# Kernel optimization log

Measured on AMD Instinct MI355X. Metric: run time of the kernel, lower is better.

## Reference

```python
import jax, jax.numpy as jnp
import numpy as np

EPS = 1e-6
NUM_HEADS = 16

def rmsnorm(x, w):
    # x: [..., d], w: [d]
    norm = jax.lax.rsqrt(jnp.mean(x * x, axis=-1, keepdims=True) + EPS)
    return w * (x * norm)

def setup_inputs() -> dict:
    key = jax.random.key(0)
    ks = jax.random.split(key, 6)
    B, N, C = 2, 2048, 1024
    H = NUM_HEADS
    hd = C // H
    x = jax.random.normal(ks[0], (B, N, C), dtype=jnp.float32)
    scale = 1.0 / np.sqrt(C)
    qkv_w = jax.random.normal(ks[1], (C, 3 * C), dtype=jnp.float32) * scale
    qkv_b = jnp.zeros((3 * C,), dtype=jnp.float32)
    q_norm_w = jnp.ones((hd,), dtype=jnp.float32)
    k_norm_w = jnp.ones((hd,), dtype=jnp.float32)
    proj_w = jax.random.normal(ks[2], (C, C), dtype=jnp.float32) * scale
    proj_b = jnp.zeros((C,), dtype=jnp.float32)
    return {"x": x, "qkv_w": qkv_w, "qkv_b": qkv_b,
            "q_norm_w": q_norm_w, "k_norm_w": k_norm_w,
            "proj_w": proj_w, "proj_b": proj_b}

def reference(x, qkv_w, qkv_b, q_norm_w, k_norm_w, proj_w, proj_b):
    B, N, C = x.shape
    H = NUM_HEADS
    hd = C // H
    qkv = x @ qkv_w + qkv_b                       # [B,N,3C]
    qkv = qkv.reshape(B, N, 3, H, hd)
    q, k, v = qkv[:, :, 0], qkv[:, :, 1], qkv[:, :, 2]  # [B,N,H,hd]
    q = jnp.transpose(q, (0, 2, 1, 3))            # [B,H,N,hd]
    k = jnp.transpose(k, (0, 2, 1, 3))
    v = jnp.transpose(v, (0, 2, 1, 3))
    q = rmsnorm(q, q_norm_w)
    k = rmsnorm(k, k_norm_w)
    scores = jnp.einsum('bhqd,bhkd->bhqk', q, k) / jnp.sqrt(jnp.float32(hd))
    attn = jax.nn.softmax(scores, axis=-1)
    out = jnp.einsum('bhqk,bhkd->bhqd', attn, v)  # [B,H,N,hd]
    out = jnp.transpose(out, (0, 2, 1, 3)).reshape(B, N, C)
    return out @ proj_w + proj_b
```

## Files before the change

### kernel.cpp

```cpp
#include <hip/hip_runtime.h>

typedef unsigned short u16;
typedef unsigned int u32;
typedef __bf16 bf16x8 __attribute__((ext_vector_type(8)));
typedef float f32x4 __attribute__((ext_vector_type(4)));
typedef unsigned short u16x8 __attribute__((ext_vector_type(8)));
typedef unsigned short u16x4 __attribute__((ext_vector_type(4)));

__device__ __forceinline__ float bf2f(u16 u) {
    union { unsigned int i; float f; } c; c.i = ((unsigned int)u) << 16; return c.f;
}
__device__ __forceinline__ u16 f2bf(float f) {
    union { float f; unsigned int i; } c; c.f = f;
    unsigned int r = c.i + 0x7FFFu + ((c.i >> 16) & 1u);
    return (u16)(r >> 16);
}
__device__ __forceinline__ u16 f2bf_rtz(float f) {
    union { float f; unsigned int i; } c; c.f = f;
    return (u16)(c.i >> 16);
}
__device__ __forceinline__ float fast_exp2(float x) {
#if __has_builtin(__builtin_amdgcn_exp2f)
    return __builtin_amdgcn_exp2f(x);
#else
    return exp2f(x);
#endif
}
__device__ __forceinline__ bf16x8 u2b(u16x8 v) {
    return __builtin_bit_cast(bf16x8, v);
}
__device__ __forceinline__ void async16(const void* g, void* l) {
    __builtin_amdgcn_global_load_lds(
        (const __attribute__((address_space(1))) u32*)g,
        (__attribute__((address_space(3))) u32*)l, 16, 0, 0);
}

__global__ __launch_bounds__(256) void prep(
    const float* __restrict__ X, u16* __restrict__ Xb,
    const float* __restrict__ qkv_w, u16* __restrict__ qwT,
    const float* __restrict__ proj_w, u16* __restrict__ pwT)
{
    __shared__ float tile[32][33];
    const int blk = blockIdx.x;
    const int t = threadIdx.x;
    if (blk < 2048) {
        const size_t i = ((size_t)blk * 256 + t) * 8;
        u16x8 h;
        #pragma unroll
        for (int e = 0; e < 8; ++e) h[e] = f2bf(X[i + e]);
        *(u16x8*)&Xb[i] = h;
        return;
    }
    const float* W; u16* Th; int K, N, bx, by;
    if (blk < 5120) {
        W = qkv_w; Th = qwT; K = 1024; N = 3072;
        bx = (blk - 2048) % 96; by = (blk - 2048) / 96;
    } else {
        W = proj_w; Th = pwT; K = 1024; N = 1024;
        bx = (blk - 5120) % 32; by = (blk - 5120) / 32;
    }
    const int bk = by * 32, bn = bx * 32;
    const int tx = t & 31, ty = t >> 5;
    #pragma unroll
    for (int r = ty; r < 32; r += 8)
        tile[r][tx] = W[(size_t)(bk + r) * N + bn + tx];
    __syncthreads();
    #pragma unroll
    for (int r = ty; r < 32; r += 8)
        Th[(size_t)(bn + r) * K + bk + tx] = f2bf(tile[tx][r]);
}

__global__ __launch_bounds__(256) void gemm_qkv(
    const u16* __restrict__ AH, const u16* __restrict__ BH,
    const float* __restrict__ bias,
    u16* __restrict__ Qb, u16* __restrict__ Kb, u16* __restrict__ Vt,
    const float* __restrict__ qw, const float* __restrict__ kw)
{
    const int K = 1024;
    __shared__ __align__(16) u16 AhT[128 * 32];
    __shared__ __align__(16) u16 BhT[128 * 32];
    const int t = threadIdx.x;
    const int bm = blockIdx.y * 128, bn = blockIdx.x * 128;
    const int wave = t >> 6, lane = t & 63;
    const int wm = (wave >> 1) * 64, wn = (wave & 1) * 64;
    const int l15 = lane & 15, quad = lane >> 4;
    const int srow = lane >> 2;
    const int scol = (((lane & 3) ^ ((lane >> 3) & 3))) * 8;
    const int rq = (quad ^ ((l15 >> 1) & 3)) * 8;

    f32x4 acc[4][4];
    const f32x4 zero = {0.0f, 0.0f, 0.0f, 0.0f};
    #pragma unroll
    for (int i = 0; i < 4; ++i)
        #pragma unroll
        for (int j = 0; j < 4; ++j) acc[i][j] = zero;

    for (int k0 = 0; k0 < K; k0 += 32) {
        #pragma unroll
        for (int rr = 0; rr < 2; ++rr) {
            const int r0 = (rr * 4 + wave) * 16;
            const size_t ga = (size_t)(bm + r0 + srow) * K + k0 + scol;
            const size_t gb = (size_t)(bn + r0 + srow) * K + k0 + scol;
            async16(&AH[ga], &AhT[r0 * 32]);
            async16(&BH[gb], &BhT[r0 * 32]);
        }
        __syncthreads();
        bf16x8 ah[4], bh[4];
        #pragma unroll
        for (int i = 0; i < 4; ++i)
            ah[i] = *(const bf16x8*)&AhT[(wm + i * 16 + l15) * 32 + rq];
        #pragma unroll
        for (int j = 0; j < 4; ++j)
            bh[j] = *(const bf16x8*)&BhT[(wn + j * 16 + l15) * 32 + rq];
        #pragma unroll
        for (int i = 0; i < 4; ++i)
            #pragma unroll
            for (int j = 0; j < 4; ++j)
                acc[i][j] = __builtin_amdgcn_mfma_f32_16x16x32_bf16(
                    ah[i], bh[j], acc[i][j], 0, 0, 0);
        __syncthreads();
    }

    const int gc0 = bn + wn;
    const int sec = gc0 >> 10;
    const int h = (gc0 & 1023) >> 6;
    const int b = bm >> 11;
    const int bhd = b * 16 + h;
    float bv[4], wj[4];
    #pragma unroll
    for (int j = 0; j < 4; ++j) {
        const int d = j * 16 + l15;
        bv[j] = bias[gc0 + d];
        wj[j] = (sec == 2) ? 0.0f : (sec ? kw[d] : qw[d] * 0.18033688011f);
    }
    if (sec < 2) {
        u16* dst = sec ? Kb : Qb;
        #pragma unroll
        for (int i = 0; i < 4; ++i) {
            float val[4][4];
            float ss[4] = {0.0f, 0.0f, 0.0f, 0.0f};
            #pragma unroll
            for (int j = 0; j < 4; ++j)
                #pragma unroll
                for (int r = 0; r < 4; ++r) {
                    val[j][r] = acc[i][j][r] + bv[j];
                    ss[r] += val[j][r] * val[j][r];
                }
            #pragma unroll
            for (int r = 0; r < 4; ++r) {
                #pragma unroll
                for (int m = 1; m < 16; m <<= 1)
                    ss[r] += __shfl_xor(ss[r], m, 64);
                const float nrm = rsqrtf(ss[r] * 0.015625f + 1e-6f);
                const int n = (bm + wm + i * 16 + quad * 4 + r) & 2047;
                const size_t rowb = ((size_t)bhd * 2048 + n) * 64;
                #pragma unroll
                for (int j = 0; j < 4; ++j)
                    dst[rowb + j * 16 + l15] = f2bf(val[j][r] * nrm * wj[j]);
            }
        }
    } else {
        const int nb = (bm + wm) & 2047;
        #pragma unroll
        for (int i = 0; i < 4; ++i) {
            const int s0 = (i & 1) * 32 + quad * 8 + (i >> 1) * 4;
            #pragma unroll
            for (int j = 0; j < 4; ++j) {
                const int d = j * 16 + l15;
                u16x4 pk;
                #pragma unroll
                for (int r = 0; r < 4; ++r)
                    pk[r] = f2bf(acc[i][j][r] + bv[j]);
                *(u16x4*)&Vt[((size_t)bhd * 64 + d) * 2048 + nb + s0] = pk;
            }
        }
    }
}

__global__ __launch_bounds__(256) void gemm_proj(
    const u16* __restrict__ AH, const u16* __restrict__ BH,
    const float* __restrict__ bias, float* __restrict__ C)
{
    const int N = 1024, K = 1024;
    __shared__ __align__(16) u16 AhT[64 * 32];
    __shared__ __align__(16) u16 BhT[128 * 32];
    const int t = threadIdx.x;
    const int bm = blockIdx.y * 64, bn = blockIdx.x * 128;
    const int wave = t >> 6, lane = t & 63;
    const int l15 = lane & 15, quad = lane >> 4;
    const int srow = lane >> 2;
    const int scol = (((lane & 3) ^ ((lane >> 3) & 3))) * 8;
    const int rq = (quad ^ ((l15 >> 1) & 3)) * 8;

    f32x4 acc[4][2];
    const f32x4 zero = {0.0f, 0.0f, 0.0f, 0.0f};
    #pragma unroll
    for (int i = 0; i < 4; ++i)
        #pragma unroll
        for (int j = 0; j < 2; ++j) acc[i][j] = zero;

    for (int k0 = 0; k0 < K; k0 += 32) {
        {
            const int r0 = wave * 16;
            async16(&AH[(size_t)(bm + r0 + srow) * K + k0 + scol],
                    &AhT[r0 * 32]);
        }
        #pragma unroll
        for (int cc = 0; cc < 2; ++cc) {
            const int r0 = (wave * 2 + cc) * 16;
            async16(&BH[(size_t)(bn + r0 + srow) * K + k0 + scol],
                    &BhT[r0 * 32]);
        }
        __syncthreads();
        bf16x8 ah[4], bh[2];
        #pragma unroll
        for (int i = 0; i < 4; ++i)
            ah[i] = *(const bf16x8*)&AhT[(i * 16 + l15) * 32 + rq];
        #pragma unroll
        for (int j = 0; j < 2; ++j)
            bh[j] = *(const bf16x8*)
                &BhT[(wave * 32 + j * 16 + l15) * 32 + rq];
        #pragma unroll
        for (int i = 0; i < 4; ++i)
            #pragma unroll
            for (int j = 0; j < 2; ++j)
                acc[i][j] = __builtin_amdgcn_mfma_f32_16x16x32_bf16(
                    ah[i], bh[j], acc[i][j], 0, 0, 0);
        __syncthreads();
    }

    #pragma unroll
    for (int j = 0; j < 2; ++j) {
        const int col = bn + wave * 32 + j * 16 + l15;
        const float bv = bias[col];
        #pragma unroll
        for (int i = 0; i < 4; ++i) {
            const int row = bm + i * 16 + quad * 4;
            #pragma unroll
            for (int r = 0; r < 4; ++r)
                C[(size_t)(row + r) * N + col] = acc[i][j][r] + bv;
        }
    }
}

__global__ __launch_bounds__(256) void flash_attn_mfma(
    const u16* __restrict__ Qb, const u16* __restrict__ Kb,
    const u16* __restrict__ Vt, u16* __restrict__ Attn)
{
    __shared__ __align__(16) u16 Klds[2 * 64 * 64];
    __shared__ __align__(16) u16 Vlds[2 * 64 * 64];

    const int t = threadIdx.x;
    const int bid = blockIdx.x;
    const int bh = bid & 31;
    const int qt = bid >> 5;
    const int n0 = qt * 128;
    const size_t kbase = (size_t)bh * 2048 * 64;
    const size_t vbase = (size_t)bh * 64 * 2048;
    const int wave = t >> 6, lane = t & 63;
    const int l15 = lane & 15, quad = lane >> 4;
    const int srow8 = lane >> 3;
    const int sgrp = lane & 7;

    bf16x8 qf[2][2];
    #pragma unroll
    for (int qs = 0; qs < 2; ++qs) {
        const size_t qrow =
            ((size_t)bh * 2048 + n0 + wave * 32 + qs * 16 + l15) * 64;
        qf[qs][0] = *(const bf16x8*)&Qb[qrow + quad * 8];
        qf[qs][1] = *(const bf16x8*)&Qb[qrow + 32 + quad * 8];
    }

    int kofs[4][2];
    #pragma unroll
    for (int nt = 0; nt < 4; ++nt) {
        const int row = nt * 16 + l15;
        kofs[nt][0] = row * 64 + ((quad ^ (row & 7)) * 8);
        kofs[nt][1] = row * 64 + (((quad + 4) ^ (row & 7)) * 8);
    }

    f32x4 o[2][4];
    const f32x4 zero = {0.0f, 0.0f, 0.0f, 0.0f};
    #pragma unroll
    for (int qs = 0; qs < 2; ++qs)
        #pragma unroll
        for (int dt = 0; dt < 4; ++dt) o[qs][dt] = zero;
    f32x4 osum[2] = {zero, zero};
    bf16x8 ones;
    #pragma unroll
    for (int e = 0; e < 8; ++e) ones[e] = (__bf16)1.0f;

    #pragma unroll
    for (int cc = 0; cc < 2; ++cc) {
        const int r0 = (wave + cc * 4) * 8;
        const int row = r0 + srow8;
        const int gg = sgrp ^ (row & 7);
        async16(&Kb[kbase + (size_t)row * 64 + gg * 8], &Klds[r0 * 64]);
        async16(&Vt[vbase + (size_t)row * 2048 + gg * 8], &Vlds[r0 * 64]);
    }

    for (int kt = 0; kt < 32; ++kt) {
        __syncthreads();
        if (kt + 1 < 32) {
            const int nb = ((kt + 1) & 1) * 4096;
            #pragma unroll
            for (int cc = 0; cc < 2; ++cc) {
                const int r0 = (wave + cc * 4) * 8;
                const int row = r0 + srow8;
                const int gg = sgrp ^ (row & 7);
                async16(&Kb[kbase + (size_t)((kt + 1) * 64 + row) * 64 + gg * 8],
                        &Klds[nb + r0 * 64]);
                async16(&Vt[vbase + (size_t)row * 2048 + (kt + 1) * 64 + gg * 8],
                        &Vlds[nb + r0 * 64]);
            }
        }
        const int cb = (kt & 1) * 4096;

        f32x4 s[2][4];
        #pragma unroll
        for (int nt = 0; nt < 4; ++nt) {
            bf16x8 kf0 = *(const bf16x8*)&Klds[cb + kofs[nt][0]];
            bf16x8 kf1 = *(const bf16x8*)&Klds[cb + kofs[nt][1]];
            __builtin_amdgcn_s_setprio(1);
            #pragma unroll
            for (int qs = 0; qs < 2; ++qs) {
                s[qs][nt] = __builtin_amdgcn_mfma_f32_16x16x32_bf16(
                    kf0, qf[qs][0], zero, 0, 0, 0);
                s[qs][nt] = __builtin_amdgcn_mfma_f32_16x16x32_bf16(
                    kf1, qf[qs][1], s[qs][nt], 0, 0, 0);
            }
            __builtin_amdgcn_s_setprio(0);
        }

        bf16x8 pf[2][2];
        #pragma unroll
        for (int qs = 0; qs < 2; ++qs) {
            #pragma unroll
            for (int m = 0; m < 2; ++m) {
                u16x8 pk;
                #pragma unroll
                for (int r = 0; r < 4; ++r) {
                    pk[r]     = f2bf_rtz(fast_exp2(s[qs][m][r]));
                    pk[4 + r] = f2bf_rtz(fast_exp2(s[qs][m + 2][r]));
                }
                pf[qs][m] = u2b(pk);
            }
        }

        #pragma unroll
        for (int dt = 0; dt < 4; ++dt) {
            bf16x8 vf0 = *(const bf16x8*)&Vlds[cb + kofs[dt][0]];
            bf16x8 vf1 = *(const bf16x8*)&Vlds[cb + kofs[dt][1]];
            __builtin_amdgcn_s_setprio(1);
            #pragma unroll
            for (int qs = 0; qs < 2; ++qs) {
                o[qs][dt] = __builtin_amdgcn_mfma_f32_16x16x32_bf16(
                    pf[qs][0], vf0, o[qs][dt], 0, 0, 0);
                o[qs][dt] = __builtin_amdgcn_mfma_f32_16x16x32_bf16(
                    pf[qs][1], vf1, o[qs][dt], 0, 0, 0);
            }
            __builtin_amdgcn_s_setprio(0);
        }
        __builtin_amdgcn_s_setprio(1);
        #pragma unroll
        for (int qs = 0; qs < 2; ++qs) {
            osum[qs] = __builtin_amdgcn_mfma_f32_16x16x32_bf16(
                pf[qs][0], ones, osum[qs], 0, 0, 0);
            osum[qs] = __builtin_amdgcn_mfma_f32_16x16x32_bf16(
                pf[qs][1], ones, osum[qs], 0, 0, 0);
        }
        __builtin_amdgcn_s_setprio(0);
    }

    const size_t obase =
        ((size_t)(bh >> 4) * 2048 + n0) * 1024 + (bh & 15) * 64;
    #pragma unroll
    for (int qs = 0; qs < 2; ++qs)
        #pragma unroll
        for (int r = 0; r < 4; ++r) {
            const float inv = 1.0f / osum[qs][r];
            const size_t rbase =
                obase + (size_t)(wave * 32 + qs * 16 + quad * 4 + r) * 1024;
            #pragma unroll
            for (int dt = 0; dt < 4; ++dt)
                Attn[rbase + dt * 16 + l15] = f2bf(o[qs][dt][r] * inv);
        }
}

extern "C" void kernel_launch(void* const* d_in, const int* in_sizes, int n_in,
                              void* d_out, int out_size, void* d_ws, size_t ws_size,
                              hipStream_t stream)
{
    const float* x      = (const float*)d_in[0];
    const float* qkv_w  = (const float*)d_in[1];
    const float* qkv_b  = (const float*)d_in[2];
    const float* q_nw   = (const float*)d_in[3];
    const float* k_nw   = (const float*)d_in[4];
    const float* proj_w = (const float*)d_in[5];
    const float* proj_b = (const float*)d_in[6];
    float* out = (float*)d_out;

    char* ws = (char*)d_ws;
    u16* AttnB = (u16*)ws;
    u16* qwT   = (u16*)(ws + 8388608);
    u16* pwT   = (u16*)(ws + 14680064);
    u16* Xb    = (u16*)(ws + 16777216);
    u16* QbB   = (u16*)(ws + 25165824);
    u16* KbB   = (u16*)(ws + 33554432);
    u16* VtB   = (u16*)(ws + 41943040);
    (void)in_sizes; (void)n_in; (void)out_size;
    if (ws_size < 50331648u) return;

    prep<<<dim3(6144), 256, 0, stream>>>(x, Xb, qkv_w, qwT, proj_w, pwT);
    gemm_qkv<<<dim3(3072 / 128, 4096 / 128), 256, 0, stream>>>(
        Xb, qwT, qkv_b, QbB, KbB, VtB, q_nw, k_nw);
    flash_attn_mfma<<<dim3(512), 256, 0, stream>>>(QbB, KbB, VtB, AttnB);
    gemm_proj<<<dim3(1024 / 128, 4096 / 64), 256, 0, stream>>>(
        AttnB, pwT, proj_b, out);
}
```

Baseline: 198.7 us.

## Double QKV GEMM k-tile to 64 and remap blocks for XCD locality

The QKV GEMM now loads 64-wide K slices per iteration into larger LDS tiles with a new XOR swizzle, halving the number of barrier pairs per K loop. It also replaces the 2D grid with a 1D grid of 768 blocks, mapping each XCD to a contiguous set of column tiles so weight tiles are more likely to be reused in that XCD's L2. The price is doubled LDS usage and more live registers for the fragments, which could lower occupancy.

```diff
diff --git a/kernel.cpp b/kernel.cpp
--- a/kernel.cpp
+++ b/kernel.cpp
@@ -77,16 +77,19 @@
     const float* __restrict__ qw, const float* __restrict__ kw)
 {
     const int K = 1024;
-    __shared__ __align__(16) u16 AhT[128 * 32];
-    __shared__ __align__(16) u16 BhT[128 * 32];
+    __shared__ __align__(16) u16 AhT[128 * 64];
+    __shared__ __align__(16) u16 BhT[128 * 64];
     const int t = threadIdx.x;
-    const int bm = blockIdx.y * 128, bn = blockIdx.x * 128;
+    const int bid = blockIdx.x;
+    const int xcd = bid & 7, slot = bid >> 3;
+    const int bm = (slot / 3) * 128;
+    const int bn = (xcd * 3 + (slot % 3)) * 128;
     const int wave = t >> 6, lane = t & 63;
     const int wm = (wave >> 1) * 64, wn = (wave & 1) * 64;
     const int l15 = lane & 15, quad = lane >> 4;
-    const int srow = lane >> 2;
-    const int scol = (((lane & 3) ^ ((lane >> 3) & 3))) * 8;
-    const int rq = (quad ^ ((l15 >> 1) & 3)) * 8;
+    const int srow_lo = lane >> 3;
+    const int g8 = ((lane & 7) ^ (lane >> 3)) * 8;
+    const int rx = l15 & 7;
 
     f32x4 acc[4][4];
     const f32x4 zero = {0.0f, 0.0f, 0.0f, 0.0f};
@@ -95,29 +98,37 @@
         #pragma unroll
         for (int j = 0; j < 4; ++j) acc[i][j] = zero;
 
-    for (int k0 = 0; k0 < K; k0 += 32) {
-        #pragma unroll
-        for (int rr = 0; rr < 2; ++rr) {
-            const int r0 = (rr * 4 + wave) * 16;
-            const size_t ga = (size_t)(bm + r0 + srow) * K + k0 + scol;
-            const size_t gb = (size_t)(bn + r0 + srow) * K + k0 + scol;
-            async16(&AH[ga], &AhT[r0 * 32]);
-            async16(&BH[gb], &BhT[r0 * 32]);
+    for (int k0 = 0; k0 < K; k0 += 64) {
+        #pragma unroll
+        for (int cc = 0; cc < 4; ++cc) {
+            const int seg = cc * 4 + wave;
+            const int row = seg * 8 + srow_lo;
+            async16(&AH[(size_t)(bm + row) * K + k0 + g8], &AhT[seg * 512]);
+            async16(&BH[(size_t)(bn + row) * K + k0 + g8], &BhT[seg * 512]);
         }
         __syncthreads();
-        bf16x8 ah[4], bh[4];
+        bf16x8 ah[4][2], bh[4][2];
+        #pragma unroll
+        for (int i = 0; i < 4; ++i) {
+            const int rb = (wm + i * 16 + l15) * 64;
+            ah[i][0] = *(const bf16x8*)&AhT[rb + (quad ^ rx) * 8];
+            ah[i][1] = *(const bf16x8*)&AhT[rb + (((4 + quad) ^ rx)) * 8];
+        }
+        #pragma unroll
+        for (int j = 0; j < 4; ++j) {
+            const int rb = (wn + j * 16 + l15) * 64;
+            bh[j][0] = *(const bf16x8*)&BhT[rb + (quad ^ rx) * 8];
+            bh[j][1] = *(const bf16x8*)&BhT[rb + (((4 + quad) ^ rx)) * 8];
+        }
         #pragma unroll
         for (int i = 0; i < 4; ++i)
-            ah[i] = *(const bf16x8*)&AhT[(wm + i * 16 + l15) * 32 + rq];
-        #pragma unroll
-        for (int j = 0; j < 4; ++j)
-            bh[j] = *(const bf16x8*)&BhT[(wn + j * 16 + l15) * 32 + rq];
-        #pragma unroll
-        for (int i = 0; i < 4; ++i)
-            #pragma unroll
-            for (int j = 0; j < 4; ++j)
+            #pragma unroll
+            for (int j = 0; j < 4; ++j) {
                 acc[i][j] = __builtin_amdgcn_mfma_f32_16x16x32_bf16(
-                    ah[i], bh[j], acc[i][j], 0, 0, 0);
+                    ah[i][0], bh[j][0], acc[i][j], 0, 0, 0);
+                acc[i][j] = __builtin_amdgcn_mfma_f32_16x16x32_bf16(
+                    ah[i][1], bh[j][1], acc[i][j], 0, 0, 0);
+            }
         __syncthreads();
     }
 
@@ -412,7 +423,7 @@
     if (ws_size < 50331648u) return;
 
     prep<<<dim3(6144), 256, 0, stream>>>(x, Xb, qkv_w, qwT, proj_w, pwT);
-    gemm_qkv<<<dim3(3072 / 128, 4096 / 128), 256, 0, stream>>>(
+    gemm_qkv<<<dim3(768), 256, 0, stream>>>(
         Xb, qwT, qkv_b, QbB, KbB, VtB, q_nw, k_nw);
     flash_attn_mfma<<<dim3(512), 256, 0, stream>>>(QbB, KbB, VtB, AttnB);
     gemm_proj<<<dim3(1024 / 128, 4096 / 64), 256, 0, stream>>>(
```

Measured after the change: 198.2 us. No clear change (-0.3%).

## Double K-step per barrier in proj GEMM and drop setprio in attention

Applied to the files above, without the earlier changes.

The projection GEMM now loads two 32-wide K slices into LDS per iteration, halving the number of __syncthreads barriers and loop iterations at the cost of double the shared memory. Separately, the s_setprio priority hints around the MFMA blocks in the flash attention kernel are removed. Both changes aim to reduce synchronization and scheduling overhead. Removing setprio may change how waves interleave memory and compute.

```diff
diff --git a/kernel.cpp b/kernel.cpp
--- a/kernel.cpp
+++ b/kernel.cpp
@@ -182,8 +182,8 @@
     const float* __restrict__ bias, float* __restrict__ C)
 {
     const int N = 1024, K = 1024;
-    __shared__ __align__(16) u16 AhT[64 * 32];
-    __shared__ __align__(16) u16 BhT[128 * 32];
+    __shared__ __align__(16) u16 AhT[2 * 64 * 32];
+    __shared__ __align__(16) u16 BhT[2 * 128 * 32];
     const int t = threadIdx.x;
     const int bm = blockIdx.y * 64, bn = blockIdx.x * 128;
     const int wave = t >> 6, lane = t & 63;
@@ -199,33 +199,41 @@
         #pragma unroll
         for (int j = 0; j < 2; ++j) acc[i][j] = zero;
 
-    for (int k0 = 0; k0 < K; k0 += 32) {
-        {
-            const int r0 = wave * 16;
-            async16(&AH[(size_t)(bm + r0 + srow) * K + k0 + scol],
-                    &AhT[r0 * 32]);
-        }
-        #pragma unroll
-        for (int cc = 0; cc < 2; ++cc) {
-            const int r0 = (wave * 2 + cc) * 16;
-            async16(&BH[(size_t)(bn + r0 + srow) * K + k0 + scol],
-                    &BhT[r0 * 32]);
+    for (int k0 = 0; k0 < K; k0 += 64) {
+        #pragma unroll
+        for (int s = 0; s < 2; ++s) {
+            const int kk = k0 + s * 32;
+            {
+                const int r0 = wave * 16;
+                async16(&AH[(size_t)(bm + r0 + srow) * K + kk + scol],
+                        &AhT[s * 2048 + r0 * 32]);
+            }
+            #pragma unroll
+            for (int cc = 0; cc < 2; ++cc) {
+                const int r0 = (wave * 2 + cc) * 16;
+                async16(&BH[(size_t)(bn + r0 + srow) * K + kk + scol],
+                        &BhT[s * 4096 + r0 * 32]);
+            }
         }
         __syncthreads();
-        bf16x8 ah[4], bh[2];
-        #pragma unroll
-        for (int i = 0; i < 4; ++i)
-            ah[i] = *(const bf16x8*)&AhT[(i * 16 + l15) * 32 + rq];
-        #pragma unroll
-        for (int j = 0; j < 2; ++j)
-            bh[j] = *(const bf16x8*)
-                &BhT[(wave * 32 + j * 16 + l15) * 32 + rq];
-        #pragma unroll
-        for (int i = 0; i < 4; ++i)
+        #pragma unroll
+        for (int s = 0; s < 2; ++s) {
+            const int ab = s * 2048, bb = s * 4096;
+            bf16x8 ah[4], bh[2];
+            #pragma unroll
+            for (int i = 0; i < 4; ++i)
+                ah[i] = *(const bf16x8*)&AhT[ab + (i * 16 + l15) * 32 + rq];
             #pragma unroll
             for (int j = 0; j < 2; ++j)
-                acc[i][j] = __builtin_amdgcn_mfma_f32_16x16x32_bf16(
-                    ah[i], bh[j], acc[i][j], 0, 0, 0);
+                bh[j] = *(const bf16x8*)
+                    &BhT[bb + (wave * 32 + j * 16 + l15) * 32 + rq];
+            #pragma unroll
+            for (int i = 0; i < 4; ++i)
+                #pragma unroll
+                for (int j = 0; j < 2; ++j)
+                    acc[i][j] = __builtin_amdgcn_mfma_f32_16x16x32_bf16(
+                        ah[i], bh[j], acc[i][j], 0, 0, 0);
+        }
         __syncthreads();
     }
 
@@ -321,7 +329,6 @@
         for (int nt = 0; nt < 4; ++nt) {
             bf16x8 kf0 = *(const bf16x8*)&Klds[cb + kofs[nt][0]];
             bf16x8 kf1 = *(const bf16x8*)&Klds[cb + kofs[nt][1]];
-            __builtin_amdgcn_s_setprio(1);
             #pragma unroll
             for (int qs = 0; qs < 2; ++qs) {
                 s[qs][nt] = __builtin_amdgcn_mfma_f32_16x16x32_bf16(
@@ -329,7 +336,6 @@
                 s[qs][nt] = __builtin_amdgcn_mfma_f32_16x16x32_bf16(
                     kf1, qf[qs][1], s[qs][nt], 0, 0, 0);
             }
-            __builtin_amdgcn_s_setprio(0);
         }
 
         bf16x8 pf[2][2];
@@ -351,7 +357,6 @@
         for (int dt = 0; dt < 4; ++dt) {
             bf16x8 vf0 = *(const bf16x8*)&Vlds[cb + kofs[dt][0]];
             bf16x8 vf1 = *(const bf16x8*)&Vlds[cb + kofs[dt][1]];
-            __builtin_amdgcn_s_setprio(1);
             #pragma unroll
             for (int qs = 0; qs < 2; ++qs) {
                 o[qs][dt] = __builtin_amdgcn_mfma_f32_16x16x32_bf16(
@@ -359,9 +364,7 @@
                 o[qs][dt] = __builtin_amdgcn_mfma_f32_16x16x32_bf16(
                     pf[qs][1], vf1, o[qs][dt], 0, 0, 0);
             }
-            __builtin_amdgcn_s_setprio(0);
-        }
-        __builtin_amdgcn_s_setprio(1);
+        }
         #pragma unroll
         for (int qs = 0; qs < 2; ++qs) {
             osum[qs] = __builtin_amdgcn_mfma_f32_16x16x32_bf16(
@@ -369,7 +372,6 @@
             osum[qs] = __builtin_amdgcn_mfma_f32_16x16x32_bf16(
                 pf[qs][1], ones, osum[qs], 0, 0, 0);
         }
-        __builtin_amdgcn_s_setprio(0);
     }
 
     const size_t obase =
```

New measurement: 190.8 us. 1.04x faster.
